# Kernel optimization log

Hardware: AMD Instinct MI355X
Metric: run time of the kernel (lower is better)

The kernel has to match this reference:

```python
import jax, jax.numpy as jnp
import numpy as np


def _lstm(x, Wx, Wh, b):
    """Fused-gate LSTM over time axis 1. x: [B,T,I]; Wx: [I,4H]; Wh: [H,4H]; b: [4H].
    Gate order (i, f, g, o) as in flax.linen.LSTMCell. Zero initial carry."""
    B, T, _ = x.shape
    H = Wh.shape[0]
    # Precompute all input-to-gate contributions in one big GEMM.
    xg = jnp.einsum('bti,ih->bth', x, Wx) + b  # [B,T,4H]

    def step(carry, xt):
        c, h = carry
        z = xt + h @ Wh  # [B,4H]
        i, f, g, o = jnp.split(z, 4, axis=-1)
        c = jax.nn.sigmoid(f) * c + jax.nn.sigmoid(i) * jnp.tanh(g)
        h = jax.nn.sigmoid(o) * jnp.tanh(c)
        return (c, h), h

    init = (jnp.zeros((B, H), x.dtype), jnp.zeros((B, H), x.dtype))
    _, hs = jax.lax.scan(step, init, jnp.swapaxes(xg, 0, 1))  # hs: [T,B,H]
    return jnp.swapaxes(hs, 0, 1)  # [B,T,H]


def _forward(X, conv_w, conv_b,
             Wx1, Wh1, b1, Wx2, Wh2, b2, Wx3, Wh3, b3, Wx4, Wh4, b4,
             Wa, ba, Va, bva, Wd1, bd1, Wd2, bd2):
    # 1-D conv, SAME padding (flax default), NWC layout.
    x = jax.lax.conv_general_dilated(X, conv_w, (1,), 'SAME',
                                     dimension_numbers=('NWC', 'WIO', 'NWC')) + conv_b
    # NOTE: source uses jnp.flip(..., axis=-1) -> flips FEATURE axis (faithful to source).
    x1 = _lstm(x, Wx1, Wh1, b1)
    x2 = _lstm(jnp.flip(x, axis=-1), Wx2, Wh2, b2)
    x = jnp.concatenate([x1, x2], axis=-1)  # [B,T,2F]
    x1 = _lstm(x, Wx3, Wh3, b3)
    x2 = _lstm(jnp.flip(x, axis=-1), Wx4, Wh4, b4)
    enc = jnp.concatenate([x1, x2], axis=-1)  # [B,T,4F]
    # Additive attention: softmax over time axis.
    score = jnp.tanh(enc @ Wa + ba) @ Va + bva  # [B,T,1]
    w = jax.nn.softmax(score, axis=1)
    ctx = jnp.sum(w * enc, axis=1)  # [B,4F]
    # MLP head (dropout deterministic -> identity).
    h = jnp.tanh(ctx @ Wd1 + bd1)
    return h @ Wd2 + bd2  # [B,1]


def setup_inputs() -> dict:
    key = jax.random.key(0)
    B, T, Cin, F = 32, 4096, 8, 64
    ks = iter(jax.random.split(key, 32))

    def w(shape):
        fan_in = shape[0] if len(shape) <= 2 else shape[0] * shape[1]
        return jax.random.normal(next(ks), shape, jnp.float32) / np.sqrt(fan_in)

    d = {}
    d['X'] = jax.random.normal(next(ks), (B, T, Cin), jnp.float32)
    d['conv_w'] = w((4, Cin, 16))
    d['conv_b'] = jnp.zeros((16,), jnp.float32)
    lstm_dims = {'1': (16, F), '2': (16, F), '3': (2 * F, 2 * F), '4': (2 * F, 2 * F)}
    for n, (i_dim, h_dim) in lstm_dims.items():
        d['Wx' + n] = w((i_dim, 4 * h_dim))
        d['Wh' + n] = w((h_dim, 4 * h_dim))
        d['b' + n] = jnp.zeros((4 * h_dim,), jnp.float32)
    d['Wa'] = w((4 * F, F)); d['ba'] = jnp.zeros((F,), jnp.float32)
    d['Va'] = w((F, 1));     d['bva'] = jnp.zeros((1,), jnp.float32)
    d['Wd1'] = w((4 * F, F)); d['bd1'] = jnp.zeros((F,), jnp.float32)
    d['Wd2'] = w((F, 1));     d['bd2'] = jnp.zeros((1,), jnp.float32)
    d['deterministic'] = 1
    return d


def reference(X, conv_w, conv_b,
              Wx1, Wh1, b1, Wx2, Wh2, b2, Wx3, Wh3, b3, Wx4, Wh4, b4,
              Wa, ba, Va, bva, Wd1, bd1, Wd2, bd2, deterministic):
    # deterministic=1 -> dropout is the identity; already reflected in _forward.
    return _forward(X, conv_w, conv_b,
                    Wx1, Wh1, b1, Wx2, Wh2, b2, Wx3, Wh3, b3, Wx4, Wh4, b4,
                    Wa, ba, Va, bva, Wd1, bd1, Wd2, bd2)
```

## Files before the change

### kernel.cpp

```cpp
#include <hip/hip_runtime.h>


#define TFULL 4096
#define NB 32

__device__ __forceinline__ float fexp2(float x){ return __builtin_amdgcn_exp2f(x); }
__device__ __forceinline__ float frcp(float x){ return __builtin_amdgcn_rcpf(x); }
__device__ __forceinline__ float sigf(float x){ return frcp(1.f + fexp2(-1.44269504f*x)); }
__device__ __forceinline__ float tanh_(float x){
    float e = fexp2(fminf(2.88539008f*x, 126.f));
    return (e - 1.f) * frcp(e + 1.f);
}

__global__ __launch_bounds__(256) void k_init(float* __restrict__ st1,
        float* __restrict__ st2, float* __restrict__ am, float* __restrict__ al,
        float* __restrict__ acc){
    int i = blockIdx.x * 256 + threadIdx.x;
    if (i < 8192)  st1[i] = 0.f;
    if (i < 16384) st2[i] = 0.f;
    if (i < 8192)  acc[i] = 0.f;
    if (i < 32){ am[i] = -3.4e38f; al[i] = 0.f; }
}

__global__ __launch_bounds__(256) void k_conv(const float* __restrict__ X,
        const float* __restrict__ W, const float* __restrict__ Bv,
        float* __restrict__ out, int t0, int lc){
    __shared__ float Ws[512];
    __shared__ float bs[16];
    int tid = threadIdx.x;
    Ws[tid] = W[tid]; Ws[tid + 256] = W[tid + 256];
    if (tid < 16) bs[tid] = Bv[tid];
    __syncthreads();
    int m = blockIdx.x * 256 + tid;
    int b = m >> lc, trel = m & ((1 << lc) - 1);
    int t = t0 + trel;
    float o[16];
    #pragma unroll
    for (int co = 0; co < 16; ++co) o[co] = bs[co];
    #pragma unroll
    for (int w = 0; w < 4; ++w){
        int tt = t + w - 1;
        if (tt >= 0 && tt < TFULL){
            const float* xr = X + ((size_t)(b << 12) + tt) * 8;
            #pragma unroll
            for (int ci = 0; ci < 8; ++ci){
                float v = xr[ci];
                #pragma unroll
                for (int co = 0; co < 16; ++co) o[co] += v * Ws[(w*8 + ci)*16 + co];
            }
        }
    }
    float* op = out + (size_t)m * 16;
    #pragma unroll
    for (int q = 0; q < 4; ++q)
        *(float4*)(op + q*4) = make_float4(o[q*4], o[q*4+1], o[q*4+2], o[q*4+3]);
}

__global__ __launch_bounds__(256) void k_scan1(const float* __restrict__ x,
        const float* __restrict__ Wx1, const float* __restrict__ Wh1, const float* __restrict__ b1,
        const float* __restrict__ Wx2, const float* __restrict__ Wh2, const float* __restrict__ b2,
        float* __restrict__ cc, float* __restrict__ st1, int C){
    int l = blockIdx.x >> 5;
    int b = blockIdx.x & 31;
    int j = threadIdx.x;
    const float* Wx = l ? Wx2 : Wx1;
    const float* Wh = l ? Wh2 : Wh1;
    const float* bb = l ? b2  : b1;
    float wx[16], wh[64];
    #pragma unroll
    for (int r = 0; r < 16; ++r) wx[r] = l ? Wx[(15 - r)*256 + j] : Wx[r*256 + j];
    #pragma unroll
    for (int k = 0; k < 64; ++k) wh[k] = Wh[k*256 + j];
    float bias = bb[j];

    __shared__ float xs[128 * 16];
    __shared__ float zbuf[256];
    __shared__ float hbuf[64];
    float c = 0.f;
    int sidx = (l*32 + b)*64 + (j & 63);
    if (j < 64){ c = st1[sidx]; hbuf[j] = st1[4096 + sidx]; }
    __syncthreads();

    const float* xb = x + ((size_t)b * C) * 16;
    float* ccb = cc + ((size_t)b * C) * 128 + (l << 6);

    for (int t = 0; t < C; ++t){
        int s = t & 127;
        if (s == 0){
            __syncthreads();
            const float4* src = (const float4*)(xb + (size_t)t * 16);
            float4* dst = (float4*)xs;
            if (t + (j >> 2) < C)          dst[j] = src[j];
            if (t + ((j + 256) >> 2) < C)  dst[j + 256] = src[j + 256];
            __syncthreads();
        }
        float z = bias;
        const float4* xr = (const float4*)(xs + s * 16);
        #pragma unroll
        for (int r4 = 0; r4 < 4; ++r4){
            float4 xv = xr[r4];
            z = fmaf(xv.x, wx[4*r4], z);   z = fmaf(xv.y, wx[4*r4+1], z);
            z = fmaf(xv.z, wx[4*r4+2], z); z = fmaf(xv.w, wx[4*r4+3], z);
        }
        const float4* hb4 = (const float4*)hbuf;
        #pragma unroll
        for (int k4 = 0; k4 < 16; ++k4){
            float4 hv = hb4[k4];
            z = fmaf(hv.x, wh[4*k4], z);   z = fmaf(hv.y, wh[4*k4+1], z);
            z = fmaf(hv.z, wh[4*k4+2], z); z = fmaf(hv.w, wh[4*k4+3], z);
        }
        zbuf[j] = z;
        __syncthreads();
        if (j < 64){
            float ig = sigf(zbuf[j]);
            float fg = sigf(zbuf[64 + j]);
            float gg = tanh_(zbuf[128 + j]);
            float og = sigf(zbuf[192 + j]);
            c = fg * c + ig * gg;
            float h = og * tanh_(c);
            hbuf[j] = h;
            ccb[(size_t)t * 128 + j] = h;
        }
        __syncthreads();
    }
    if (j < 64){ st1[sidx] = c; st1[4096 + sidx] = hbuf[j]; }
}

__global__ __launch_bounds__(256) void k_pack34(const float* __restrict__ Wx3,
        const float* __restrict__ Wx4, const float* __restrict__ b3, const float* __restrict__ b4,
        float* __restrict__ W34, float* __restrict__ b34){
    int e = blockIdx.x * 256 + threadIdx.x;
    int k = e >> 10, n = e & 1023;
    W34[e] = (n < 512) ? Wx3[k*512 + n] : Wx4[(127 - k)*512 + (n - 512)];
    if (e < 1024) b34[e] = (e < 512) ? b3[e] : b4[e - 512];
}

template<bool TANH>
__global__ __launch_bounds__(128) void k_gemm(
        const float* __restrict__ A, int lda,
        const float* __restrict__ B, int ldb,
        const float* __restrict__ bias,
        float* __restrict__ Cm, int ldc, int K){
    __shared__ float As[64 * 129];
    __shared__ float Bs[64 * 68];
    int tid = threadIdx.x;
    int tx = tid & 7;
    int ty = tid >> 3;
    int r0 = blockIdx.x * 128;
    int n0 = blockIdx.y * 64;
    float acc[8][8];
    #pragma unroll
    for (int i = 0; i < 8; ++i)
        #pragma unroll
        for (int n = 0; n < 8; ++n) acc[i][n] = 0.f;

    for (int kb = 0; kb < K; kb += 64){
        __syncthreads();
        for (int idx = tid; idx < 2048; idx += 128){
            int r = idx >> 4, k4 = idx & 15;
            float4 v = *(const float4*)(A + (size_t)(r0 + r) * lda + kb + k4*4);
            As[(k4*4 + 0)*129 + r] = v.x;
            As[(k4*4 + 1)*129 + r] = v.y;
            As[(k4*4 + 2)*129 + r] = v.z;
            As[(k4*4 + 3)*129 + r] = v.w;
        }
        for (int idx = tid; idx < 1024; idx += 128){
            int n4 = idx & 15, k = idx >> 4;
            float4 v = *(const float4*)(B + (size_t)(kb + k) * ldb + n0 + n4*4);
            *(float4*)(Bs + k*68 + n4*4) = v;
        }
        __syncthreads();
        #pragma unroll 4
        for (int k = 0; k < 64; ++k){
            float a[8];
            #pragma unroll
            for (int i = 0; i < 8; ++i) a[i] = As[k*129 + ty*8 + i];
            float4 b0 = *(const float4*)(Bs + k*68 + tx*8);
            float4 b1 = *(const float4*)(Bs + k*68 + tx*8 + 4);
            float bq[8] = {b0.x, b0.y, b0.z, b0.w, b1.x, b1.y, b1.z, b1.w};
            #pragma unroll
            for (int i = 0; i < 8; ++i)
                #pragma unroll
                for (int n = 0; n < 8; ++n) acc[i][n] += a[i] * bq[n];
        }
    }
    #pragma unroll
    for (int i = 0; i < 8; ++i){
        size_t rr = (size_t)r0 + ty*8 + i;
        float* cp = Cm + rr * ldc + n0 + tx*8;
        float ov[8];
        #pragma unroll
        for (int n = 0; n < 8; ++n){
            float v = acc[i][n] + bias[n0 + tx*8 + n];
            ov[n] = TANH ? tanh_(v) : v;
        }
        *(float4*)cp       = make_float4(ov[0], ov[1], ov[2], ov[3]);
        *(float4*)(cp + 4) = make_float4(ov[4], ov[5], ov[6], ov[7]);
    }
}

__global__ __launch_bounds__(512) void k_scan2(const float* __restrict__ xg,
        const float* __restrict__ Wh3, const float* __restrict__ Wh4,
        float* __restrict__ enc, float* __restrict__ st2, int C){
    int l = blockIdx.x >> 5;
    int b = blockIdx.x & 31;
    int j = threadIdx.x;
    const float* Wh = l ? Wh4 : Wh3;
    float wh[128];
    #pragma unroll
    for (int k = 0; k < 128; ++k) wh[k] = Wh[k*512 + j];

    __shared__ float zbuf[512];
    __shared__ float hbuf[128];
    float c = 0.f;
    int sidx = (l*32 + b)*128 + (j & 127);
    if (j < 128){ c = st2[sidx]; hbuf[j] = st2[8192 + sidx]; }
    __syncthreads();

    const float* xp = xg + ((size_t)b * C) * 1024 + (l << 9) + j;
    float* encb = enc + ((size_t)b * C) * 256 + (l << 7);

    float xnext = xp[0];
    for (int t = 0; t < C; ++t){
        float z = xnext;
        int tn = (t + 1 < C) ? t + 1 : t;
        xnext = xp[(size_t)tn * 1024];
        const float4* hb4 = (const float4*)hbuf;
        #pragma unroll
        for (int k4 = 0; k4 < 32; ++k4){
            float4 hv = hb4[k4];
            z = fmaf(hv.x, wh[4*k4], z);   z = fmaf(hv.y, wh[4*k4+1], z);
            z = fmaf(hv.z, wh[4*k4+2], z); z = fmaf(hv.w, wh[4*k4+3], z);
        }
        zbuf[j] = z;
        __syncthreads();
        if (j < 128){
            float ig = sigf(zbuf[j]);
            float fg = sigf(zbuf[128 + j]);
            float gg = tanh_(zbuf[256 + j]);
            float og = sigf(zbuf[384 + j]);
            c = fg * c + ig * gg;
            float h = og * tanh_(c);
            hbuf[j] = h;
            encb[(size_t)t * 256 + j] = h;
        }
        __syncthreads();
    }
    if (j < 128){ st2[sidx] = c; st2[8192 + sidx] = hbuf[j]; }
}

__global__ __launch_bounds__(256) void k_scorev(const float* __restrict__ u,
        const float* __restrict__ Va, const float* __restrict__ bva,
        float* __restrict__ sc){
    int m = blockIdx.x * 256 + threadIdx.x;
    const float4* up = (const float4*)(u + (size_t)m * 64);
    const float4* vp = (const float4*)Va;
    float acc = 0.f;
    #pragma unroll
    for (int i = 0; i < 16; ++i){
        float4 v = up[i], w = vp[i];
        acc += v.x*w.x + v.y*w.y + v.z*w.z + v.w*w.w;
    }
    sc[m] = acc + bva[0];
}

__global__ __launch_bounds__(256) void k_attn(const float* __restrict__ sc,
        const float* __restrict__ enc, float* __restrict__ am,
        float* __restrict__ al, float* __restrict__ acc, int C){
    int b = blockIdx.x, tid = threadIdx.x;
    __shared__ float es[1024];
    __shared__ float red[4];
    __shared__ float sh[2];
    const float* sp = sc + (size_t)b * C;
    float mloc = -3.4e38f;
    for (int t = tid; t < C; t += 256) mloc = fmaxf(mloc, sp[t]);
    #pragma unroll
    for (int off = 32; off; off >>= 1) mloc = fmaxf(mloc, __shfl_down(mloc, off));
    if ((tid & 63) == 0) red[tid >> 6] = mloc;
    __syncthreads();
    if (tid == 0){
        float mc = fmaxf(fmaxf(red[0], red[1]), fmaxf(red[2], red[3]));
        float mo = am[b];
        float mn = fmaxf(mo, mc);
        sh[0] = mn;
        sh[1] = fexp2(1.44269504f * (mo - mn));
        am[b] = mn;
    }
    __syncthreads();
    float mn = sh[0], alpha = sh[1];
    float eloc = 0.f;
    for (int t = tid; t < C; t += 256){
        float e = fexp2(1.44269504f * (sp[t] - mn));
        es[t] = e; eloc += e;
    }
    #pragma unroll
    for (int off = 32; off; off >>= 1) eloc += __shfl_down(eloc, off);
    if ((tid & 63) == 0) red[tid >> 6] = eloc;
    __syncthreads();
    if (tid == 0) al[b] = al[b] * alpha + (red[0] + red[1] + red[2] + red[3]);
    const float* ep = enc + (size_t)b * C * 256 + tid;
    float a = acc[b*256 + tid] * alpha;
    for (int t = 0; t < C; ++t) a += es[t] * ep[(size_t)t * 256];
    acc[b*256 + tid] = a;
}

__global__ __launch_bounds__(256) void k_head(const float* __restrict__ acc,
        const float* __restrict__ al,
        const float* __restrict__ Wd1, const float* __restrict__ bd1,
        const float* __restrict__ Wd2, const float* __restrict__ bd2,
        float* __restrict__ out){
    __shared__ float ctxs[32 * 256];
    __shared__ float h1s[32 * 64];
    int tid = threadIdx.x;
    for (int idx = tid; idx < 8192; idx += 256){
        int b = idx >> 8;
        ctxs[idx] = acc[idx] / al[b];
    }
    __syncthreads();
    for (int idx = tid; idx < 2048; idx += 256){
        int b = idx >> 6, n = idx & 63;
        float a = bd1[n];
        for (int i = 0; i < 256; ++i) a += ctxs[b*256 + i] * Wd1[i*64 + n];
        h1s[idx] = tanh_(a);
    }
    __syncthreads();
    if (tid < 32){
        float a = bd2[0];
        #pragma unroll
        for (int n = 0; n < 64; ++n) a += h1s[tid*64 + n] * Wd2[n];
        out[tid] = a;
    }
}

extern "C" void kernel_launch(void* const* d_in, const int* in_sizes, int n_in,
                              void* d_out, int out_size, void* d_ws, size_t ws_size,
                              hipStream_t stream){
    const float* X     = (const float*)d_in[0];
    const float* convw = (const float*)d_in[1];
    const float* convb = (const float*)d_in[2];
    const float* Wx1 = (const float*)d_in[3];
    const float* Wh1 = (const float*)d_in[4];
    const float* b1  = (const float*)d_in[5];
    const float* Wx2 = (const float*)d_in[6];
    const float* Wh2 = (const float*)d_in[7];
    const float* b2  = (const float*)d_in[8];
    const float* Wx3 = (const float*)d_in[9];
    const float* Wh3 = (const float*)d_in[10];
    const float* b3  = (const float*)d_in[11];
    const float* Wx4 = (const float*)d_in[12];
    const float* Wh4 = (const float*)d_in[13];
    const float* b4  = (const float*)d_in[14];
    const float* Wa  = (const float*)d_in[15];
    const float* ba  = (const float*)d_in[16];
    const float* Va  = (const float*)d_in[17];
    const float* bva = (const float*)d_in[18];
    const float* Wd1 = (const float*)d_in[19];
    const float* bd1 = (const float*)d_in[20];
    const float* Wd2 = (const float*)d_in[21];
    const float* bd2 = (const float*)d_in[22];
    float* out = (float*)d_out;
    (void)in_sizes; (void)n_in; (void)out_size;

    const size_t fixedFl = 131072 + 1024 + 8192 + 16384 + 32 + 32 + 8192 + 32*1024;
    size_t capFl = ws_size / 4;
    int C = 1024;
    while (C > 32){
        size_t need = fixedFl + (size_t)NB * C * (16 + 128 + 1024 + 256 + 64);
        if (need <= capFl) break;
        C >>= 1;
    }
    int lc = 31 - __builtin_clz((unsigned)C);
    int nch = TFULL / C;

    float* ws  = (float*)d_ws;
    float* W34 = ws;
    float* b34 = W34 + 131072;
    float* st1 = b34 + 1024;
    float* st2 = st1 + 8192;
    float* am  = st2 + 16384;
    float* al  = am + 32;
    float* acc = al + 32;
    float* scb = acc + 8192;
    float* xcv = scb + 32*1024;
    float* ccb = xcv + (size_t)NB*C*16;
    float* xgb = ccb + (size_t)NB*C*128;
    float* enb = xgb + (size_t)NB*C*1024;
    float* ub  = enb + (size_t)NB*C*256;

    k_init<<<64, 256, 0, stream>>>(st1, st2, am, al, acc);
    k_pack34<<<512, 256, 0, stream>>>(Wx3, Wx4, b3, b4, W34, b34);

    for (int ch = 0; ch < nch; ++ch){
        int t0 = ch * C;
        k_conv<<<NB*C/256, 256, 0, stream>>>(X, convw, convb, xcv, t0, lc);
        k_scan1<<<64, 256, 0, stream>>>(xcv, Wx1, Wh1, b1, Wx2, Wh2, b2, ccb, st1, C);
        k_gemm<false><<<dim3(NB*C/128, 16), 128, 0, stream>>>(
            ccb, 128, W34, 1024, b34, xgb, 1024, 128);
        k_scan2<<<64, 512, 0, stream>>>(xgb, Wh3, Wh4, enb, st2, C);
        k_gemm<true><<<dim3(NB*C/128, 1), 128, 0, stream>>>(
            enb, 256, Wa, 64, ba, ub, 64, 256);
        k_scorev<<<NB*C/256, 256, 0, stream>>>(ub, Va, bva, scb);
        k_attn<<<32, 256, 0, stream>>>(scb, enb, am, al, acc, C);
    }
    k_head<<<1, 256, 0, stream>>>(acc, al, Wd1, bd1, Wd2, bd2, out);
}
```

Before: 6.628 ms.

## Split recurrent K-reduction across two thread halves and parallelize attention over time

Both LSTM scan kernels now double the thread count and split the hidden-state dot product across two halves, with partial sums combined in shared memory before the gate nonlinearities. This shortens the serial FMA chain per time step, and four independent accumulators add ILP. The attention kernel moves to 1024 threads and splits the time loop into four slices reduced at the end. The cost is higher per-block thread and register demand plus an extra shared-memory add per gate.

```diff
diff --git a/kernel.cpp b/kernel.cpp
--- a/kernel.cpp
+++ b/kernel.cpp
@@ -56,29 +56,36 @@
         *(float4*)(op + q*4) = make_float4(o[q*4], o[q*4+1], o[q*4+2], o[q*4+3]);
 }
 
-__global__ __launch_bounds__(256) void k_scan1(const float* __restrict__ x,
+__global__ __launch_bounds__(512) void k_scan1(const float* __restrict__ x,
         const float* __restrict__ Wx1, const float* __restrict__ Wh1, const float* __restrict__ b1,
         const float* __restrict__ Wx2, const float* __restrict__ Wh2, const float* __restrict__ b2,
         float* __restrict__ cc, float* __restrict__ st1, int C){
     int l = blockIdx.x >> 5;
     int b = blockIdx.x & 31;
     int j = threadIdx.x;
+    int col = j & 255;
+    int half = j >> 8;
     const float* Wx = l ? Wx2 : Wx1;
     const float* Wh = l ? Wh2 : Wh1;
     const float* bb = l ? b2  : b1;
-    float wx[16], wh[64];
-    #pragma unroll
-    for (int r = 0; r < 16; ++r) wx[r] = l ? Wx[(15 - r)*256 + j] : Wx[r*256 + j];
-    #pragma unroll
-    for (int k = 0; k < 64; ++k) wh[k] = Wh[k*256 + j];
-    float bias = bb[j];
+    float wx[16], wh[32], bias = 0.f;
+    if (half == 0){
+        #pragma unroll
+        for (int r = 0; r < 16; ++r) wx[r] = l ? Wx[(15 - r)*256 + col] : Wx[r*256 + col];
+        bias = bb[col];
+    } else {
+        #pragma unroll
+        for (int r = 0; r < 16; ++r) wx[r] = 0.f;
+    }
+    #pragma unroll
+    for (int k = 0; k < 32; ++k) wh[k] = Wh[(half*32 + k)*256 + col];
 
     __shared__ float xs[128 * 16];
-    __shared__ float zbuf[256];
-    __shared__ float hbuf[64];
+    __shared__ float zp[512];
+    __shared__ float hbufs[64];
     float c = 0.f;
     int sidx = (l*32 + b)*64 + (j & 63);
-    if (j < 64){ c = st1[sidx]; hbuf[j] = st1[4096 + sidx]; }
+    if (j < 64){ c = st1[sidx]; hbufs[j] = st1[4096 + sidx]; }
     __syncthreads();
 
     const float* xb = x + ((size_t)b * C) * 16;
@@ -90,40 +97,45 @@
             __syncthreads();
             const float4* src = (const float4*)(xb + (size_t)t * 16);
             float4* dst = (float4*)xs;
-            if (t + (j >> 2) < C)          dst[j] = src[j];
-            if (t + ((j + 256) >> 2) < C)  dst[j + 256] = src[j + 256];
+            if (t + (j >> 2) < C) dst[j] = src[j];
             __syncthreads();
         }
-        float z = bias;
-        const float4* xr = (const float4*)(xs + s * 16);
-        #pragma unroll
-        for (int r4 = 0; r4 < 4; ++r4){
-            float4 xv = xr[r4];
-            z = fmaf(xv.x, wx[4*r4], z);   z = fmaf(xv.y, wx[4*r4+1], z);
-            z = fmaf(xv.z, wx[4*r4+2], z); z = fmaf(xv.w, wx[4*r4+3], z);
-        }
-        const float4* hb4 = (const float4*)hbuf;
-        #pragma unroll
-        for (int k4 = 0; k4 < 16; ++k4){
-            float4 hv = hb4[k4];
-            z = fmaf(hv.x, wh[4*k4], z);   z = fmaf(hv.y, wh[4*k4+1], z);
-            z = fmaf(hv.z, wh[4*k4+2], z); z = fmaf(hv.w, wh[4*k4+3], z);
-        }
-        zbuf[j] = z;
+        float a0 = bias, a1 = 0.f, a2 = 0.f, a3 = 0.f;
+        if (half == 0){
+            const float4* xr = (const float4*)(xs + s * 16);
+            #pragma unroll
+            for (int r4 = 0; r4 < 4; ++r4){
+                float4 xv = xr[r4];
+                a0 = fmaf(xv.x, wx[4*r4+0], a0);
+                a1 = fmaf(xv.y, wx[4*r4+1], a1);
+                a2 = fmaf(xv.z, wx[4*r4+2], a2);
+                a3 = fmaf(xv.w, wx[4*r4+3], a3);
+            }
+        }
+        const float4* hb4 = (const float4*)hbufs;
+        #pragma unroll
+        for (int k4 = 0; k4 < 8; ++k4){
+            float4 hv = hb4[(half << 3) + k4];
+            a0 = fmaf(hv.x, wh[4*k4+0], a0);
+            a1 = fmaf(hv.y, wh[4*k4+1], a1);
+            a2 = fmaf(hv.z, wh[4*k4+2], a2);
+            a3 = fmaf(hv.w, wh[4*k4+3], a3);
+        }
+        zp[(half << 8) + col] = (a0 + a1) + (a2 + a3);
         __syncthreads();
         if (j < 64){
-            float ig = sigf(zbuf[j]);
-            float fg = sigf(zbuf[64 + j]);
-            float gg = tanh_(zbuf[128 + j]);
-            float og = sigf(zbuf[192 + j]);
-            c = fg * c + ig * gg;
-            float h = og * tanh_(c);
-            hbuf[j] = h;
+            float zi = zp[j]       + zp[256 + j];
+            float zf = zp[64 + j]  + zp[320 + j];
+            float zg = zp[128 + j] + zp[384 + j];
+            float zo = zp[192 + j] + zp[448 + j];
+            c = sigf(zf) * c + sigf(zi) * tanh_(zg);
+            float h = sigf(zo) * tanh_(c);
+            hbufs[j] = h;
             ccb[(size_t)t * 128 + j] = h;
         }
         __syncthreads();
     }
-    if (j < 64){ st1[sidx] = c; st1[4096 + sidx] = hbuf[j]; }
+    if (j < 64){ st1[sidx] = c; st1[4096 + sidx] = hbufs[j]; }
 }
 
 __global__ __launch_bounds__(256) void k_pack34(const float* __restrict__ Wx3,
@@ -199,54 +211,62 @@
     }
 }
 
-__global__ __launch_bounds__(512) void k_scan2(const float* __restrict__ xg,
+__global__ __launch_bounds__(1024, 4) void k_scan2(const float* __restrict__ xg,
         const float* __restrict__ Wh3, const float* __restrict__ Wh4,
         float* __restrict__ enc, float* __restrict__ st2, int C){
     int l = blockIdx.x >> 5;
     int b = blockIdx.x & 31;
     int j = threadIdx.x;
+    int col = j & 511;
+    int half = j >> 9;
     const float* Wh = l ? Wh4 : Wh3;
-    float wh[128];
-    #pragma unroll
-    for (int k = 0; k < 128; ++k) wh[k] = Wh[k*512 + j];
-
-    __shared__ float zbuf[512];
-    __shared__ float hbuf[128];
+    float wh[64];
+    #pragma unroll
+    for (int k = 0; k < 64; ++k) wh[k] = Wh[(half*64 + k)*512 + col];
+
+    __shared__ float zp[1024];
+    __shared__ float hbufs[128];
     float c = 0.f;
     int sidx = (l*32 + b)*128 + (j & 127);
-    if (j < 128){ c = st2[sidx]; hbuf[j] = st2[8192 + sidx]; }
-    __syncthreads();
-
-    const float* xp = xg + ((size_t)b * C) * 1024 + (l << 9) + j;
+    if (j < 128){ c = st2[sidx]; hbufs[j] = st2[8192 + sidx]; }
+    __syncthreads();
+
+    const float* xp = xg + ((size_t)b * C) * 1024 + (l << 9) + col;
     float* encb = enc + ((size_t)b * C) * 256 + (l << 7);
 
-    float xnext = xp[0];
+    float xnext = (half == 0) ? xp[0] : 0.f;
     for (int t = 0; t < C; ++t){
-        float z = xnext;
-        int tn = (t + 1 < C) ? t + 1 : t;
-        xnext = xp[(size_t)tn * 1024];
-        const float4* hb4 = (const float4*)hbuf;
-        #pragma unroll
-        for (int k4 = 0; k4 < 32; ++k4){
-            float4 hv = hb4[k4];
-            z = fmaf(hv.x, wh[4*k4], z);   z = fmaf(hv.y, wh[4*k4+1], z);
-            z = fmaf(hv.z, wh[4*k4+2], z); z = fmaf(hv.w, wh[4*k4+3], z);
-        }
-        zbuf[j] = z;
+        float a0 = 0.f, a1 = 0.f, a2 = 0.f, a3 = 0.f;
+        const float4* hb4 = (const float4*)hbufs;
+        #pragma unroll
+        for (int k4 = 0; k4 < 16; ++k4){
+            float4 hv = hb4[(half << 4) + k4];
+            a0 = fmaf(hv.x, wh[4*k4+0], a0);
+            a1 = fmaf(hv.y, wh[4*k4+1], a1);
+            a2 = fmaf(hv.z, wh[4*k4+2], a2);
+            a3 = fmaf(hv.w, wh[4*k4+3], a3);
+        }
+        float z = (a0 + a1) + (a2 + a3);
+        if (half == 0){
+            z += xnext;
+            int tn = (t + 1 < C) ? t + 1 : t;
+            xnext = xp[(size_t)tn * 1024];
+        }
+        zp[(half << 9) + col] = z;
         __syncthreads();
         if (j < 128){
-            float ig = sigf(zbuf[j]);
-            float fg = sigf(zbuf[128 + j]);
-            float gg = tanh_(zbuf[256 + j]);
-            float og = sigf(zbuf[384 + j]);
-            c = fg * c + ig * gg;
-            float h = og * tanh_(c);
-            hbuf[j] = h;
+            float zi = zp[j]        + zp[512 + j];
+            float zf = zp[128 + j]  + zp[640 + j];
+            float zg = zp[256 + j]  + zp[768 + j];
+            float zo = zp[384 + j]  + zp[896 + j];
+            c = sigf(zf) * c + sigf(zi) * tanh_(zg);
+            float h = sigf(zo) * tanh_(c);
+            hbufs[j] = h;
             encb[(size_t)t * 256 + j] = h;
         }
         __syncthreads();
     }
-    if (j < 128){ st2[sidx] = c; st2[8192 + sidx] = hbuf[j]; }
+    if (j < 128){ st2[sidx] = c; st2[8192 + sidx] = hbufs[j]; }
 }
 
 __global__ __launch_bounds__(256) void k_scorev(const float* __restrict__ u,
@@ -264,22 +284,24 @@
     sc[m] = acc + bva[0];
 }
 
-__global__ __launch_bounds__(256) void k_attn(const float* __restrict__ sc,
+__global__ __launch_bounds__(1024) void k_attn(const float* __restrict__ sc,
         const float* __restrict__ enc, float* __restrict__ am,
         float* __restrict__ al, float* __restrict__ acc, int C){
     int b = blockIdx.x, tid = threadIdx.x;
     __shared__ float es[1024];
-    __shared__ float red[4];
+    __shared__ float red[16];
     __shared__ float sh[2];
     const float* sp = sc + (size_t)b * C;
     float mloc = -3.4e38f;
-    for (int t = tid; t < C; t += 256) mloc = fmaxf(mloc, sp[t]);
+    for (int t = tid; t < C; t += 1024) mloc = fmaxf(mloc, sp[t]);
     #pragma unroll
     for (int off = 32; off; off >>= 1) mloc = fmaxf(mloc, __shfl_down(mloc, off));
     if ((tid & 63) == 0) red[tid >> 6] = mloc;
     __syncthreads();
     if (tid == 0){
-        float mc = fmaxf(fmaxf(red[0], red[1]), fmaxf(red[2], red[3]));
+        float mc = -3.4e38f;
+        #pragma unroll
+        for (int i = 0; i < 16; ++i) mc = fmaxf(mc, red[i]);
         float mo = am[b];
         float mn = fmaxf(mo, mc);
         sh[0] = mn;
@@ -289,7 +311,7 @@
     __syncthreads();
     float mn = sh[0], alpha = sh[1];
     float eloc = 0.f;
-    for (int t = tid; t < C; t += 256){
+    for (int t = tid; t < C; t += 1024){
         float e = fexp2(1.44269504f * (sp[t] - mn));
         es[t] = e; eloc += e;
     }
@@ -297,11 +319,24 @@
     for (int off = 32; off; off >>= 1) eloc += __shfl_down(eloc, off);
     if ((tid & 63) == 0) red[tid >> 6] = eloc;
     __syncthreads();
-    if (tid == 0) al[b] = al[b] * alpha + (red[0] + red[1] + red[2] + red[3]);
-    const float* ep = enc + (size_t)b * C * 256 + tid;
-    float a = acc[b*256 + tid] * alpha;
-    for (int t = 0; t < C; ++t) a += es[t] * ep[(size_t)t * 256];
-    acc[b*256 + tid] = a;
+    if (tid == 0){
+        float s = 0.f;
+        #pragma unroll
+        for (int i = 0; i < 16; ++i) s += red[i];
+        al[b] = al[b] * alpha + s;
+    }
+    int jf = tid & 255, sl = tid >> 8;
+    int tlen = C >> 2;
+    const float* ep = enc + ((size_t)b * C + (size_t)sl * tlen) * 256 + jf;
+    const float* eb = es + sl * tlen;
+    float a = 0.f;
+    for (int t = 0; t < tlen; ++t) a = fmaf(eb[t], ep[(size_t)t * 256], a);
+    __syncthreads();
+    es[tid] = a;
+    __syncthreads();
+    if (tid < 256)
+        acc[b*256 + tid] = acc[b*256 + tid] * alpha
+                         + ((es[tid] + es[256 + tid]) + (es[512 + tid] + es[768 + tid]));
 }
 
 __global__ __launch_bounds__(256) void k_head(const float* __restrict__ acc,
@@ -393,14 +428,14 @@
     for (int ch = 0; ch < nch; ++ch){
         int t0 = ch * C;
         k_conv<<<NB*C/256, 256, 0, stream>>>(X, convw, convb, xcv, t0, lc);
-        k_scan1<<<64, 256, 0, stream>>>(xcv, Wx1, Wh1, b1, Wx2, Wh2, b2, ccb, st1, C);
+        k_scan1<<<64, 512, 0, stream>>>(xcv, Wx1, Wh1, b1, Wx2, Wh2, b2, ccb, st1, C);
         k_gemm<false><<<dim3(NB*C/128, 16), 128, 0, stream>>>(
             ccb, 128, W34, 1024, b34, xgb, 1024, 128);
-        k_scan2<<<64, 512, 0, stream>>>(xgb, Wh3, Wh4, enb, st2, C);
+        k_scan2<<<64, 1024, 0, stream>>>(xgb, Wh3, Wh4, enb, st2, C);
         k_gemm<true><<<dim3(NB*C/128, 1), 128, 0, stream>>>(
             enb, 256, Wa, 64, ba, ub, 64, 256);
         k_scorev<<<NB*C/256, 256, 0, stream>>>(ub, Va, bva, scb);
-        k_attn<<<32, 256, 0, stream>>>(scb, enb, am, al, acc, C);
+        k_attn<<<32, 1024, 0, stream>>>(scb, enb, am, al, acc, C);
     }
     k_head<<<1, 256, 0, stream>>>(acc, al, Wd1, bd1, Wd2, bd2, out);
 }
```

After: 6.359 ms. 1.04x faster.
